# Kernel optimization log

Measured on AMD Instinct MI355X. Metric: run time of the kernel, lower is better.

Reference implementation:

```python
import jax, jax.numpy as jnp
import numpy as np

B, C_IN, C_OUT, N, L = 4, 128, 256, 4096, 4
D = C_OUT // 4
EPS_BN = 1e-5


def setup_inputs() -> dict:
    key = jax.random.key(0)
    ks = jax.random.split(key, 16)
    s_in = 1.0 / np.sqrt(C_IN)
    s_out = 1.0 / np.sqrt(C_OUT)
    return {
        "features": jax.random.normal(ks[0], (B, C_IN, N), dtype=jnp.float32),
        # LBR: conv1x1 -> BN -> ReLU -> conv1x1 -> BN -> ReLU
        "lbr_w1": jax.random.uniform(ks[1], (C_OUT, C_IN), jnp.float32, -s_in, s_in),
        "lbr_g1": jnp.ones((C_OUT,), jnp.float32),
        "lbr_b1": jnp.zeros((C_OUT,), jnp.float32),
        "lbr_w2": jax.random.uniform(ks[2], (C_OUT, C_OUT), jnp.float32, -s_out, s_out),
        "lbr_g2": jnp.ones((C_OUT,), jnp.float32),
        "lbr_b2": jnp.zeros((C_OUT,), jnp.float32),
        # per-layer OffsetAttention params (stacked on leading L axis)
        # q_conv and k_conv share the same weight (q_conv.weight = k_conv.weight)
        "attn_qk_w": jax.random.uniform(ks[3], (L, D, C_OUT), jnp.float32, -s_out, s_out),
        "attn_v_w": jax.random.uniform(ks[4], (L, C_OUT, C_OUT), jnp.float32, -s_out, s_out),
        "attn_v_b": jax.random.uniform(ks[5], (L, C_OUT), jnp.float32, -s_out, s_out),
        "attn_t_w": jax.random.uniform(ks[6], (L, C_OUT, C_OUT), jnp.float32, -s_out, s_out),
        "attn_t_b": jax.random.uniform(ks[7], (L, C_OUT), jnp.float32, -s_out, s_out),
        "attn_bn_g": jnp.ones((L, C_OUT), jnp.float32),
        "attn_bn_b": jnp.zeros((L, C_OUT), jnp.float32),
    }


def batchnorm1d(x, gamma, beta):
    # x: [B, C, N]; training-mode BN: batch stats over (B, N), biased variance
    mean = jnp.mean(x, axis=(0, 2), keepdims=True)
    var = jnp.mean(jnp.square(x - mean), axis=(0, 2), keepdims=True)
    xn = (x - mean) * jax.lax.rsqrt(var + EPS_BN)
    return xn * gamma[None, :, None] + beta[None, :, None]


def offset_attention(x, qk_w, v_w, v_b, t_w, t_b, bn_g, bn_b):
    # x: [B, C, N]
    K = jnp.einsum("dc,bcn->bdn", qk_w, x)            # [B, D, N]
    # Q = same conv, permuted to [B, N, D]; attention_map = Q @ K -> [B, N, N]
    attn = jnp.einsum("bdn,bdm->bnm", K, K)
    attn = jax.nn.softmax(attn, axis=-1)
    # extra L1 renorm over dim=1 (column-wise)
    attn = attn / (1e-9 + jnp.sum(attn, axis=1, keepdims=True))
    V = jnp.einsum("dc,bcn->bdn", v_w, x) + v_b[None, :, None]  # [B, C, N]
    new_feat = jnp.einsum("bcn,bnm->bcm", V, attn)    # [B, C, N]
    off = x - new_feat
    t = jnp.einsum("dc,bcn->bdn", t_w, off) + t_b[None, :, None]
    return jax.nn.relu(batchnorm1d(t, bn_g, bn_b))


def reference(features, lbr_w1, lbr_g1, lbr_b1, lbr_w2, lbr_g2, lbr_b2,
              attn_qk_w, attn_v_w, attn_v_b, attn_t_w, attn_t_b,
              attn_bn_g, attn_bn_b):
    # LBR stem
    h = jnp.einsum("dc,bcn->bdn", lbr_w1, features)
    h = jax.nn.relu(batchnorm1d(h, lbr_g1, lbr_b1))
    h = jnp.einsum("dc,bcn->bdn", lbr_w2, h)
    h = jax.nn.relu(batchnorm1d(h, lbr_g2, lbr_b2))
    # stacked offset attention; output concatenates attention outputs only
    outs = []
    cur = h
    for i in range(L):
        cur = offset_attention(cur, attn_qk_w[i], attn_v_w[i], attn_v_b[i],
                               attn_t_w[i], attn_t_b[i], attn_bn_g[i], attn_bn_b[i])
        outs.append(cur)
    return jnp.concatenate(outs, axis=1)  # [B, C_OUT*L, N]
```

## Files before the change

kernel.cpp:

```cpp
#include <hip/hip_runtime.h>
#include <hip/hip_bf16.h>
#include <math.h>

#define NPTS 4096
#define CO   256
#define CI   128
#define BB   4
#define DQ   64
#define LL   4
#define PST  136

typedef __attribute__((ext_vector_type(8))) short bf16x8;
typedef __attribute__((ext_vector_type(4))) float f32x4;

#define MFMA16(a,b,c) __builtin_amdgcn_mfma_f32_16x16x32_bf16((a),(b),(c),0,0,0)

__device__ __forceinline__ short fb(float x) {
  __hip_bfloat16 h = __float2bfloat16(x);
  return __builtin_bit_cast(short, h);
}
__device__ __forceinline__ float bf(short s) {
  unsigned u = ((unsigned)(unsigned short)s) << 16;
  return __builtin_bit_cast(float, u);
}

__global__ __launch_bounds__(256) void cvtw_k(
    const float* __restrict__ S, short* __restrict__ D, int n8)
{
  const int i = blockIdx.x * 256 + threadIdx.x;
  if (i < n8) {
    const float4 a = ((const float4*)S)[i * 2];
    const float4 b = ((const float4*)S)[i * 2 + 1];
    bf16x8 r;
    r[0] = fb(a.x); r[1] = fb(a.y); r[2] = fb(a.z); r[3] = fb(a.w);
    r[4] = fb(b.x); r[5] = fb(b.y); r[6] = fb(b.z); r[7] = fb(b.w);
    ((bf16x8*)D)[i] = r;
  }
}

__global__ __launch_bounds__(256) void tcvt_k(
    const float* __restrict__ X, long xbs, int C, short* __restrict__ XT)
{
  const int n0 = blockIdx.x * 64, c0 = blockIdx.y * 64, b = blockIdx.z;
  const int t = threadIdx.x, tl = t & 63, tg = t >> 6;
  __shared__ float xs[64][65];
#pragma unroll
  for (int r = 0; r < 16; ++r) {
    const int cc = tg * 16 + r;
    xs[cc][tl] = X[(long)b * xbs + (long)(c0 + cc) * NPTS + n0 + tl];
  }
  __syncthreads();
#pragma unroll
  for (int r = 0; r < 16; ++r) {
    const int nn = tg * 16 + r;
    XT[((long)b * NPTS + n0 + nn) * C + c0 + tl] = fb(xs[tl][nn]);
  }
}

template<int OMODE, bool BIAS>
__global__ __launch_bounds__(256) void conv_a(
    const short* __restrict__ XT, int C,
    const short* __restrict__ Wb, const float* __restrict__ bias,
    void* __restrict__ Yv, long ybs)
{
  const int n0 = blockIdx.x * 128, d0 = blockIdx.y * 64, b = blockIdx.z;
  const int tid = threadIdx.x, w = tid >> 6, l = tid & 63, lg = l >> 4, lr = l & 15;
  const short* xb = XT + (long)b * NPTS * C;
  f32x4 acc[8];
#pragma unroll
  for (int i = 0; i < 8; ++i) acc[i] = (f32x4){0.f, 0.f, 0.f, 0.f};
  const int dr = d0 + w * 16 + lr;
  for (int kc = 0; kc < C; kc += 32) {
    const bf16x8 af = *(const bf16x8*)&Wb[(long)dr * C + kc + lg * 8];
#pragma unroll
    for (int ni = 0; ni < 8; ++ni) {
      const bf16x8 bx = *(const bf16x8*)&xb[(long)(n0 + ni * 16 + lr) * C + kc + lg * 8];
      acc[ni] = MFMA16(af, bx, acc[ni]);
    }
  }
  float bv[4] = {0.f, 0.f, 0.f, 0.f};
  if (BIAS) {
    const float4 b4 = *(const float4*)&bias[d0 + w * 16 + lg * 4];
    bv[0] = b4.x; bv[1] = b4.y; bv[2] = b4.z; bv[3] = b4.w;
  }
  const int db = d0 + w * 16 + lg * 4;
#pragma unroll
  for (int ni = 0; ni < 8; ++ni) {
    const int n = n0 + ni * 16 + lr;
#pragma unroll
    for (int j = 0; j < 4; ++j) {
      const float o = acc[ni][j] + bv[j];
      if constexpr (OMODE == 0) {
        ((float*)Yv)[(long)b * ybs + (long)(db + j) * NPTS + n] = o;
      } else {
        ((short*)Yv)[(long)b * ybs + ((long)(n0 >> 7) * CO + db + j) * 128 + (n & 127)] = fb(o);
      }
    }
  }
}

__global__ __launch_bounds__(256) void conv_b(
    const short* __restrict__ XT, const short* __restrict__ Wb,
    short* __restrict__ KTo)
{
  const int n0 = blockIdx.x * 64, b = blockIdx.y;
  const int tid = threadIdx.x, w = tid >> 6, l = tid & 63, lg = l >> 4, lr = l & 15;
  const short* xb = XT + (long)b * NPTS * CO;
  f32x4 acc[4];
#pragma unroll
  for (int i = 0; i < 4; ++i) acc[i] = (f32x4){0.f, 0.f, 0.f, 0.f};
  const long nr = n0 + w * 16 + lr;
  for (int kc = 0; kc < CO; kc += 32) {
    const bf16x8 af = *(const bf16x8*)&xb[nr * CO + kc + lg * 8];
#pragma unroll
    for (int di = 0; di < 4; ++di) {
      const bf16x8 wf = *(const bf16x8*)&Wb[(long)(di * 16 + lr) * CO + kc + lg * 8];
      acc[di] = MFMA16(af, wf, acc[di]);
    }
  }
  short* Ko = KTo + (long)b * NPTS * DQ;
  const int nb = n0 + w * 16 + lg * 4;
#pragma unroll
  for (int j = 0; j < 4; ++j) {
#pragma unroll
    for (int di = 0; di < 4; ++di)
      Ko[(long)(nb + j) * DQ + di * 16 + lr] = fb(acc[di][j]);
  }
}

__global__ __launch_bounds__(256) void bnstats_k(
    const float* __restrict__ X, long xbs,
    float* __restrict__ mean, float* __restrict__ rstd)
{
  const int c = blockIdx.x, t = threadIdx.x;
  float s = 0.f, s2 = 0.f;
  for (int b = 0; b < BB; ++b) {
    const float4* p = (const float4*)(X + (long)b * xbs + (long)c * NPTS);
    for (int n = t; n < NPTS / 4; n += 256) {
      const float4 v = p[n];
      s  += v.x + v.y + v.z + v.w;
      s2 += v.x * v.x + v.y * v.y + v.z * v.z + v.w * v.w;
    }
  }
#pragma unroll
  for (int o = 32; o > 0; o >>= 1) { s += __shfl_down(s, o); s2 += __shfl_down(s2, o); }
  __shared__ float a1[4], a2[4];
  if ((t & 63) == 0) { a1[t >> 6] = s; a2[t >> 6] = s2; }
  __syncthreads();
  if (t == 0) {
    const float S  = a1[0] + a1[1] + a1[2] + a1[3];
    const float S2 = a2[0] + a2[1] + a2[2] + a2[3];
    const float m  = S / (float)(BB * NPTS);
    const float v  = S2 / (float)(BB * NPTS) - m * m;
    mean[c] = m;
    rstd[c] = rsqrtf(v + 1e-5f);
  }
}

template<bool WF32, bool WBF>
__global__ __launch_bounds__(256) void bnrelu_t(
    const float* __restrict__ X, long xbs,
    const float* __restrict__ mean, const float* __restrict__ rstd,
    const float* __restrict__ g, const float* __restrict__ be,
    float* __restrict__ Yf, long ybs, short* __restrict__ XT)
{
  const int n0 = blockIdx.x * 64, c0 = blockIdx.y * 64, b = blockIdx.z;
  const int t = threadIdx.x, tl = t & 63, tg = t >> 6;
  __shared__ float xs[64][65];
#pragma unroll
  for (int r = 0; r < 16; ++r) {
    const int cc = tg * 16 + r, c = c0 + cc;
    float v = X[(long)b * xbs + (long)c * NPTS + n0 + tl];
    v = fmaxf((v - mean[c]) * rstd[c] * g[c] + be[c], 0.f);
    if (WF32) Yf[(long)b * ybs + (long)c * NPTS + n0 + tl] = v;
    xs[cc][tl] = v;
  }
  __syncthreads();
  if (WBF) {
#pragma unroll
    for (int r = 0; r < 16; ++r) {
      const int nn = tg * 16 + r;
      XT[((long)b * NPTS + n0 + nn) * CO + c0 + tl] = fb(xs[tl][nn]);
    }
  }
}

#define ONL(MX, SM, SV) { const float m2_ = fmaxf(MX, SV); \
  SM = SM * __expf(MX - m2_) + __expf(SV - m2_); MX = m2_; }
#define MRG(MX, SM, OFF) { const float om_ = __shfl_xor(MX, OFF); \
  const float os_ = __shfl_xor(SM, OFF); \
  const float m2_ = fmaxf(MX, om_); \
  SM = SM * __expf(MX - m2_) + os_ * __expf(om_ - m2_); MX = m2_; }

__global__ __launch_bounds__(256) void rowstats_mfma(
    const short* __restrict__ KT, float* __restrict__ pmax, float* __restrict__ psum)
{
  const int bid = blockIdx.x;
  const int b = (bid >> 1) & 3;
  const int idx = (bid >> 3) * 2 + (bid & 1);
  const int n0 = (idx & 63) * 64;
  const int chunk = idx >> 6;
  const int tid = threadIdx.x, w = tid >> 6, l = tid & 63, lg = l >> 4, lr = l & 15;
  const short* Kb = KT + (long)b * NPTS * DQ;
  const int nr = n0 + w * 16 + lr;
  const bf16x8 a0 = *(const bf16x8*)&Kb[(long)nr * DQ + lg * 8];
  const bf16x8 a1 = *(const bf16x8*)&Kb[(long)nr * DQ + 32 + lg * 8];

  float mx0 = -INFINITY, mx1 = -INFINITY, mx2 = -INFINITY, mx3 = -INFINITY;
  float sm0 = 0.f, sm1 = 0.f, sm2 = 0.f, sm3 = 0.f;

  const int mc = chunk * (NPTS / 4);
  for (int m0 = mc; m0 < mc + NPTS / 4; m0 += 16) {
    const bf16x8 b0 = *(const bf16x8*)&Kb[(long)(m0 + lr) * DQ + lg * 8];
    const bf16x8 b1 = *(const bf16x8*)&Kb[(long)(m0 + lr) * DQ + 32 + lg * 8];
    f32x4 s = {0.f, 0.f, 0.f, 0.f};
    s = MFMA16(a0, b0, s);
    s = MFMA16(a1, b1, s);
    ONL(mx0, sm0, s[0]); ONL(mx1, sm1, s[1]);
    ONL(mx2, sm2, s[2]); ONL(mx3, sm3, s[3]);
  }
#pragma unroll
  for (int off = 1; off < 16; off <<= 1) {
    MRG(mx0, sm0, off); MRG(mx1, sm1, off);
    MRG(mx2, sm2, off); MRG(mx3, sm3, off);
  }
  if (lr == 0) {
    const long base = ((long)chunk * BB + b) * NPTS + n0 + w * 16 + lg * 4;
    pmax[base + 0] = mx0; pmax[base + 1] = mx1; pmax[base + 2] = mx2; pmax[base + 3] = mx3;
    psum[base + 0] = sm0; psum[base + 1] = sm1; psum[base + 2] = sm2; psum[base + 3] = sm3;
  }
}

__global__ __launch_bounds__(256) void combine_k(
    const float* __restrict__ pmax, const float* __restrict__ psum,
    float* __restrict__ rmax, float* __restrict__ rinv)
{
  const long i = (long)blockIdx.x * 256 + threadIdx.x;
  const long st = (long)BB * NPTS;
  float m = pmax[i];
  m = fmaxf(m, pmax[st + i]); m = fmaxf(m, pmax[2 * st + i]); m = fmaxf(m, pmax[3 * st + i]);
  const float s = psum[i] * __expf(pmax[i] - m)
                + psum[st + i] * __expf(pmax[st + i] - m)
                + psum[2 * st + i] * __expf(pmax[2 * st + i] - m)
                + psum[3 * st + i] * __expf(pmax[3 * st + i] - m);
  rmax[i] = m;
  rinv[i] = 1.f / s;
}

__global__ __launch_bounds__(512) void pass2_mfma(
    const short* __restrict__ KT, const short* __restrict__ Vblk,
    const float* __restrict__ rmax, const float* __restrict__ rinv,
    short* __restrict__ XO)
{
  const int bid = blockIdx.x;
  const int b  = (bid >> 1) & 3;
  const int m0 = ((bid >> 3) * 2 + (bid & 1)) * 64;
  const int tid = threadIdx.x;
  const int w = tid >> 6, l = tid & 63, lg = l >> 4, lr = l & 15;

  const short* Kb = KT + (long)b * NPTS * DQ;
  const short* Vb = Vblk + (long)b * CO * NPTS;
  const float* rmb = rmax + (long)b * NPTS;
  const float* rib = rinv + (long)b * NPTS;

  __shared__ short Ps[2][64][PST];
  __shared__ float cspart[8][64];
  __shared__ float csum[64];

  bf16x8 bK[4][2];
#pragma unroll
  for (int ms = 0; ms < 4; ++ms) {
    bK[ms][0] = *(const bf16x8*)&Kb[(long)(m0 + ms * 16 + lr) * DQ + lg * 8];
    bK[ms][1] = *(const bf16x8*)&Kb[(long)(m0 + ms * 16 + lr) * DQ + 32 + lg * 8];
  }

  f32x4 acc[4][2];
#pragma unroll
  for (int i = 0; i < 4; ++i) {
    acc[i][0] = (f32x4){0.f, 0.f, 0.f, 0.f};
    acc[i][1] = (f32x4){0.f, 0.f, 0.f, 0.f};
  }
  float cs[4] = {0.f, 0.f, 0.f, 0.f};
  const int c0 = w * 32;
  const int nb = w * 16;

  bf16x8 a0 = *(const bf16x8*)&Kb[(long)(nb + lr) * DQ + lg * 8];
  bf16x8 a1 = *(const bf16x8*)&Kb[(long)(nb + lr) * DQ + 32 + lg * 8];
  float4 rm4 = *(const float4*)&rmb[nb + lg * 4];
  float4 ri4 = *(const float4*)&rib[nb + lg * 4];

  int buf = 0;
  for (int n0 = 0; n0 < NPTS; n0 += 128) {
    const short* vt = Vb + (long)(n0 >> 7) * CO * 128;
    bf16x8 vf[4][2];
#pragma unroll
    for (int kc = 0; kc < 4; ++kc) {
      vf[kc][0] = *(const bf16x8*)&vt[(long)(c0 + lr) * 128 + kc * 32 + lg * 8];
      vf[kc][1] = *(const bf16x8*)&vt[(long)(c0 + 16 + lr) * 128 + kc * 32 + lg * 8];
    }
    f32x4 s[4];
#pragma unroll
    for (int ms = 0; ms < 4; ++ms) {
      s[ms] = (f32x4){0.f, 0.f, 0.f, 0.f};
      s[ms] = MFMA16(a0, bK[ms][0], s[ms]);
      s[ms] = MFMA16(a1, bK[ms][1], s[ms]);
    }
#pragma unroll
    for (int ms = 0; ms < 4; ++ms) {
      const float p0 = __expf(s[ms][0] - rm4.x) * ri4.x;
      const float p1 = __expf(s[ms][1] - rm4.y) * ri4.y;
      const float p2 = __expf(s[ms][2] - rm4.z) * ri4.z;
      const float p3 = __expf(s[ms][3] - rm4.w) * ri4.w;
      cs[ms] += p0 + p1 + p2 + p3;
      const unsigned u0 = ((unsigned)(unsigned short)fb(p1) << 16) | (unsigned short)fb(p0);
      const unsigned u1 = ((unsigned)(unsigned short)fb(p3) << 16) | (unsigned short)fb(p2);
      *(uint2*)&Ps[buf][ms * 16 + lr][nb + lg * 4] = make_uint2(u0, u1);
    }
    asm volatile("s_waitcnt lgkmcnt(0)" ::: "memory");
    __builtin_amdgcn_s_barrier();
    if (n0 + 128 < NPTS) {
      a0 = *(const bf16x8*)&Kb[(long)(n0 + 128 + nb + lr) * DQ + lg * 8];
      a1 = *(const bf16x8*)&Kb[(long)(n0 + 128 + nb + lr) * DQ + 32 + lg * 8];
      rm4 = *(const float4*)&rmb[n0 + 128 + nb + lg * 4];
      ri4 = *(const float4*)&rib[n0 + 128 + nb + lg * 4];
    }
#pragma unroll
    for (int kc = 0; kc < 4; ++kc) {
      bf16x8 pa[4];
#pragma unroll
      for (int ms = 0; ms < 4; ++ms)
        pa[ms] = *(const bf16x8*)&Ps[buf][ms * 16 + lr][kc * 32 + lg * 8];
#pragma unroll
      for (int ms = 0; ms < 4; ++ms) {
        acc[ms][0] = MFMA16(pa[ms], vf[kc][0], acc[ms][0]);
        acc[ms][1] = MFMA16(pa[ms], vf[kc][1], acc[ms][1]);
      }
    }
    buf ^= 1;
  }

  __syncthreads();
#pragma unroll
  for (int ms = 0; ms < 4; ++ms) {
    float csv = cs[ms];
    csv += __shfl_xor(csv, 16); csv += __shfl_xor(csv, 32);
    if (lg == 0) cspart[w][ms * 16 + lr] = csv;
  }
  __syncthreads();
  if (tid < 64) {
    float s = 0.f;
#pragma unroll
    for (int ww = 0; ww < 8; ++ww) s += cspart[ww][tid];
    csum[tid] = s;
  }
  __syncthreads();

  short* XOb = XO + (long)b * NPTS * CO;
#pragma unroll
  for (int ms = 0; ms < 4; ++ms) {
#pragma unroll
    for (int j = 0; j < 4; ++j) {
      const int m = m0 + ms * 16 + lg * 4 + j;
      const float inv = 1.f / (1e-9f + csum[ms * 16 + lg * 4 + j]);
      const long i0 = (long)m * CO + c0 + lr;
      const long i1 = (long)m * CO + c0 + 16 + lr;
      XOb[i0] = fb(bf(XOb[i0]) - acc[ms][0][j] * inv);
      XOb[i1] = fb(bf(XOb[i1]) - acc[ms][1][j] * inv);
    }
  }
}

extern "C" void kernel_launch(void* const* d_in, const int* in_sizes, int n_in,
                              void* d_out, int out_size, void* d_ws, size_t ws_size,
                              hipStream_t stream)
{
  const float* feat = (const float*)d_in[0];
  const float* w1   = (const float*)d_in[1];
  const float* g1   = (const float*)d_in[2];
  const float* b1   = (const float*)d_in[3];
  const float* w2   = (const float*)d_in[4];
  const float* g2   = (const float*)d_in[5];
  const float* b2   = (const float*)d_in[6];
  const float* qkw  = (const float*)d_in[7];
  const float* vw   = (const float*)d_in[8];
  const float* vb   = (const float*)d_in[9];
  const float* tw   = (const float*)d_in[10];
  const float* tb   = (const float*)d_in[11];
  const float* bng  = (const float*)d_in[12];
  const float* bnb  = (const float*)d_in[13];

  float* out = (float*)d_out;

  short* xt    = (short*)d_ws;
  short* KTb   = xt + (long)BB * NPTS * CO;
  short* Vblk  = KTb + (long)BB * NPTS * DQ;
  short* wb1   = Vblk + (long)BB * CO * NPTS;
  short* wb2   = wb1 + (long)CO * CI;
  short* wqk   = wb2 + (long)CO * CO;
  short* wv    = wqk + (long)LL * DQ * CO;
  short* wt    = wv + (long)LL * CO * CO;
  float* pmaxb = (float*)(wt + (long)LL * CO * CO);
  float* psumb = pmaxb + (long)4 * BB * NPTS;
  float* rmaxb = psumb + (long)4 * BB * NPTS;
  float* rinvb = rmaxb + (long)BB * NPTS;
  float* meanb = rinvb + (long)BB * NPTS;
  float* rstdb = meanb + CO;

  const long OBS = (long)LL * CO * NPTS;
  float* h1 = out + (long)2 * CO * NPTS;
  float* x0 = out + (long)1 * CO * NPTS;

  const dim3 blk(256);

  cvtw_k<<<dim3((CO * CI / 8 + 255) / 256), blk, 0, stream>>>(w1, wb1, CO * CI / 8);
  cvtw_k<<<dim3((CO * CO / 8 + 255) / 256), blk, 0, stream>>>(w2, wb2, CO * CO / 8);
  cvtw_k<<<dim3((LL * DQ * CO / 8 + 255) / 256), blk, 0, stream>>>(qkw, wqk, LL * DQ * CO / 8);
  cvtw_k<<<dim3((LL * CO * CO / 8 + 255) / 256), blk, 0, stream>>>(vw, wv, LL * CO * CO / 8);
  cvtw_k<<<dim3((LL * CO * CO / 8 + 255) / 256), blk, 0, stream>>>(tw, wt, LL * CO * CO / 8);

  tcvt_k<<<dim3(64, 2, BB), blk, 0, stream>>>(feat, (long)CI * NPTS, CI, xt);
  conv_a<0, false><<<dim3(32, 4, BB), blk, 0, stream>>>(xt, CI, wb1, nullptr, h1, OBS);
  bnstats_k<<<dim3(CO), blk, 0, stream>>>(h1, OBS, meanb, rstdb);
  bnrelu_t<false, true><<<dim3(64, 4, BB), blk, 0, stream>>>(
      h1, OBS, meanb, rstdb, g1, b1, nullptr, 0, xt);
  conv_a<0, false><<<dim3(32, 4, BB), blk, 0, stream>>>(xt, CO, wb2, nullptr, x0, OBS);
  bnstats_k<<<dim3(CO), blk, 0, stream>>>(x0, OBS, meanb, rstdb);
  bnrelu_t<false, true><<<dim3(64, 4, BB), blk, 0, stream>>>(
      x0, OBS, meanb, rstdb, g2, b2, nullptr, 0, xt);

  for (int lyr = 0; lyr < LL; ++lyr) {
    float* nft = out + (long)lyr * CO * NPTS;
    conv_b<<<dim3(64, BB), blk, 0, stream>>>(xt, wqk + (long)lyr * DQ * CO, KTb);
    conv_a<1, true><<<dim3(32, 4, BB), blk, 0, stream>>>(
        xt, CO, wv + (long)lyr * CO * CO, vb + (long)lyr * CO, Vblk, (long)CO * NPTS);
    rowstats_mfma<<<dim3(1024), blk, 0, stream>>>(KTb, pmaxb, psumb);
    combine_k<<<dim3(BB * NPTS / 256), blk, 0, stream>>>(pmaxb, psumb, rmaxb, rinvb);
    pass2_mfma<<<dim3(256), dim3(512), 0, stream>>>(KTb, Vblk, rmaxb, rinvb, xt);
    conv_a<0, true><<<dim3(32, 4, BB), blk, 0, stream>>>(
        xt, CO, wt + (long)lyr * CO * CO, tb + (long)lyr * CO, nft, OBS);
    bnstats_k<<<dim3(CO), blk, 0, stream>>>(nft, OBS, meanb, rstdb);
    if (lyr < LL - 1) {
      bnrelu_t<true, true><<<dim3(64, 4, BB), blk, 0, stream>>>(
          nft, OBS, meanb, rstdb, bng + (long)lyr * CO, bnb + (long)lyr * CO, nft, OBS, xt);
    } else {
      bnrelu_t<true, false><<<dim3(64, 4, BB), blk, 0, stream>>>(
          nft, OBS, meanb, rstdb, bng + (long)lyr * CO, bnb + (long)lyr * CO, nft, OBS, nullptr);
    }
  }
}
```

Baseline: 911.2 us.

## Fuse BN stats into conv epilogue, bf16 intermediates, two-pass rowstats, merged weight cast

Merges the five weight-conversion launches into one kernel. The 1x1 conv now writes its pre-BN output as bf16 into scratch and accumulates per-channel sum and sum-of-squares partials in its epilogue. A small finisher kernel reduces those partials, replacing the full-tensor bnstats pass. The conv tile is halved to 64 points to give more blocks. The row-softmax statistics kernel switches from online max/sum to two passes, recomputing QK^T to drop the per-element rescale exps. This trades extra MFMA work and bf16 rounding of pre-BN values for less memory traffic and fewer launches.

```diff
diff --git a/kernel.cpp b/kernel.cpp
--- a/kernel.cpp
+++ b/kernel.cpp
@@ -24,18 +24,27 @@
   return __builtin_bit_cast(float, u);
 }
 
-__global__ __launch_bounds__(256) void cvtw_k(
-    const float* __restrict__ S, short* __restrict__ D, int n8)
-{
-  const int i = blockIdx.x * 256 + threadIdx.x;
-  if (i < n8) {
-    const float4 a = ((const float4*)S)[i * 2];
-    const float4 b = ((const float4*)S)[i * 2 + 1];
-    bf16x8 r;
-    r[0] = fb(a.x); r[1] = fb(a.y); r[2] = fb(a.z); r[3] = fb(a.w);
-    r[4] = fb(b.x); r[5] = fb(b.y); r[6] = fb(b.z); r[7] = fb(b.w);
-    ((bf16x8*)D)[i] = r;
-  }
+__global__ __launch_bounds__(256) void cvt5_k(
+    const float* __restrict__ s1, short* __restrict__ d1, int n1,
+    const float* __restrict__ s2, short* __restrict__ d2, int n2,
+    const float* __restrict__ s3, short* __restrict__ d3, int n3,
+    const float* __restrict__ s4, short* __restrict__ d4, int n4,
+    const float* __restrict__ s5, short* __restrict__ d5, int n5)
+{
+  int i = blockIdx.x * 256 + threadIdx.x;
+  const float* S; short* D;
+  if      (i < n1)                       { S = s1; D = d1; }
+  else if ((i -= n1) < n2)               { S = s2; D = d2; }
+  else if ((i -= n2) < n3)               { S = s3; D = d3; }
+  else if ((i -= n3) < n4)               { S = s4; D = d4; }
+  else if ((i -= n4) < n5)               { S = s5; D = d5; }
+  else return;
+  const float4 a = ((const float4*)S)[i * 2];
+  const float4 b = ((const float4*)S)[i * 2 + 1];
+  bf16x8 r;
+  r[0] = fb(a.x); r[1] = fb(a.y); r[2] = fb(a.z); r[3] = fb(a.w);
+  r[4] = fb(b.x); r[5] = fb(b.y); r[6] = fb(b.z); r[7] = fb(b.w);
+  ((bf16x8*)D)[i] = r;
 }
 
 __global__ __launch_bounds__(256) void tcvt_k(
@@ -61,19 +70,20 @@
 __global__ __launch_bounds__(256) void conv_a(
     const short* __restrict__ XT, int C,
     const short* __restrict__ Wb, const float* __restrict__ bias,
-    void* __restrict__ Yv, long ybs)
-{
-  const int n0 = blockIdx.x * 128, d0 = blockIdx.y * 64, b = blockIdx.z;
+    short* __restrict__ Yv, long ybs,
+    float* __restrict__ ps1, float* __restrict__ ps2)
+{
+  const int n0 = blockIdx.x * 64, d0 = blockIdx.y * 64, b = blockIdx.z;
   const int tid = threadIdx.x, w = tid >> 6, l = tid & 63, lg = l >> 4, lr = l & 15;
   const short* xb = XT + (long)b * NPTS * C;
-  f32x4 acc[8];
-#pragma unroll
-  for (int i = 0; i < 8; ++i) acc[i] = (f32x4){0.f, 0.f, 0.f, 0.f};
+  f32x4 acc[4];
+#pragma unroll
+  for (int i = 0; i < 4; ++i) acc[i] = (f32x4){0.f, 0.f, 0.f, 0.f};
   const int dr = d0 + w * 16 + lr;
   for (int kc = 0; kc < C; kc += 32) {
     const bf16x8 af = *(const bf16x8*)&Wb[(long)dr * C + kc + lg * 8];
 #pragma unroll
-    for (int ni = 0; ni < 8; ++ni) {
+    for (int ni = 0; ni < 4; ++ni) {
       const bf16x8 bx = *(const bf16x8*)&xb[(long)(n0 + ni * 16 + lr) * C + kc + lg * 8];
       acc[ni] = MFMA16(af, bx, acc[ni]);
     }
@@ -84,16 +94,39 @@
     bv[0] = b4.x; bv[1] = b4.y; bv[2] = b4.z; bv[3] = b4.w;
   }
   const int db = d0 + w * 16 + lg * 4;
-#pragma unroll
-  for (int ni = 0; ni < 8; ++ni) {
+  float s1[4], s2[4];
+#pragma unroll
+  for (int j = 0; j < 4; ++j) { s1[j] = 0.f; s2[j] = 0.f; }
+#pragma unroll
+  for (int ni = 0; ni < 4; ++ni) {
     const int n = n0 + ni * 16 + lr;
 #pragma unroll
     for (int j = 0; j < 4; ++j) {
-      const float o = acc[ni][j] + bv[j];
-      if constexpr (OMODE == 0) {
-        ((float*)Yv)[(long)b * ybs + (long)(db + j) * NPTS + n] = o;
+      const short ob = fb(acc[ni][j] + bv[j]);
+      if constexpr (OMODE == 1) {
+        Yv[(long)b * ybs + ((long)(n >> 7) * CO + db + j) * 128 + (n & 127)] = ob;
       } else {
-        ((short*)Yv)[(long)b * ybs + ((long)(n0 >> 7) * CO + db + j) * 128 + (n & 127)] = fb(o);
+        Yv[(long)b * ybs + (long)(db + j) * NPTS + n] = ob;
+        const float o = bf(ob);
+        s1[j] += o; s2[j] += o * o;
+      }
+    }
+  }
+  if constexpr (OMODE == 2) {
+#pragma unroll
+    for (int j = 0; j < 4; ++j) {
+#pragma unroll
+      for (int off = 1; off < 16; off <<= 1) {
+        s1[j] += __shfl_xor(s1[j], off);
+        s2[j] += __shfl_xor(s2[j], off);
+      }
+    }
+    if (lr == 0) {
+      const int slot = b * 64 + blockIdx.x;
+#pragma unroll
+      for (int j = 0; j < 4; ++j) {
+        ps1[(long)(db + j) * 256 + slot] = s1[j];
+        ps2[(long)(db + j) * 256 + slot] = s2[j];
       }
     }
   }
@@ -128,30 +161,22 @@
   }
 }
 
-__global__ __launch_bounds__(256) void bnstats_k(
-    const float* __restrict__ X, long xbs,
+__global__ __launch_bounds__(64) void bnfin_k(
+    const float* __restrict__ ps1, const float* __restrict__ ps2,
     float* __restrict__ mean, float* __restrict__ rstd)
 {
   const int c = blockIdx.x, t = threadIdx.x;
   float s = 0.f, s2 = 0.f;
-  for (int b = 0; b < BB; ++b) {
-    const float4* p = (const float4*)(X + (long)b * xbs + (long)c * NPTS);
-    for (int n = t; n < NPTS / 4; n += 256) {
-      const float4 v = p[n];
-      s  += v.x + v.y + v.z + v.w;
-      s2 += v.x * v.x + v.y * v.y + v.z * v.z + v.w * v.w;
-    }
+#pragma unroll
+  for (int i = 0; i < 4; ++i) {
+    s  += ps1[(long)c * 256 + t + i * 64];
+    s2 += ps2[(long)c * 256 + t + i * 64];
   }
 #pragma unroll
   for (int o = 32; o > 0; o >>= 1) { s += __shfl_down(s, o); s2 += __shfl_down(s2, o); }
-  __shared__ float a1[4], a2[4];
-  if ((t & 63) == 0) { a1[t >> 6] = s; a2[t >> 6] = s2; }
-  __syncthreads();
   if (t == 0) {
-    const float S  = a1[0] + a1[1] + a1[2] + a1[3];
-    const float S2 = a2[0] + a2[1] + a2[2] + a2[3];
-    const float m  = S / (float)(BB * NPTS);
-    const float v  = S2 / (float)(BB * NPTS) - m * m;
+    const float m = s / (float)(BB * NPTS);
+    const float v = s2 / (float)(BB * NPTS) - m * m;
     mean[c] = m;
     rstd[c] = rsqrtf(v + 1e-5f);
   }
@@ -159,7 +184,7 @@
 
 template<bool WF32, bool WBF>
 __global__ __launch_bounds__(256) void bnrelu_t(
-    const float* __restrict__ X, long xbs,
+    const short* __restrict__ X, long xbs,
     const float* __restrict__ mean, const float* __restrict__ rstd,
     const float* __restrict__ g, const float* __restrict__ be,
     float* __restrict__ Yf, long ybs, short* __restrict__ XT)
@@ -170,7 +195,7 @@
 #pragma unroll
   for (int r = 0; r < 16; ++r) {
     const int cc = tg * 16 + r, c = c0 + cc;
-    float v = X[(long)b * xbs + (long)c * NPTS + n0 + tl];
+    float v = bf(X[(long)b * xbs + (long)c * NPTS + n0 + tl]);
     v = fmaxf((v - mean[c]) * rstd[c] * g[c] + be[c], 0.f);
     if (WF32) Yf[(long)b * ybs + (long)c * NPTS + n0 + tl] = v;
     xs[cc][tl] = v;
@@ -184,13 +209,6 @@
     }
   }
 }
-
-#define ONL(MX, SM, SV) { const float m2_ = fmaxf(MX, SV); \
-  SM = SM * __expf(MX - m2_) + __expf(SV - m2_); MX = m2_; }
-#define MRG(MX, SM, OFF) { const float om_ = __shfl_xor(MX, OFF); \
-  const float os_ = __shfl_xor(SM, OFF); \
-  const float m2_ = fmaxf(MX, om_); \
-  SM = SM * __expf(MX - m2_) + os_ * __expf(om_ - m2_); MX = m2_; }
 
 __global__ __launch_bounds__(256) void rowstats_mfma(
     const short* __restrict__ KT, float* __restrict__ pmax, float* __restrict__ psum)
@@ -205,29 +223,56 @@
   const int nr = n0 + w * 16 + lr;
   const bf16x8 a0 = *(const bf16x8*)&Kb[(long)nr * DQ + lg * 8];
   const bf16x8 a1 = *(const bf16x8*)&Kb[(long)nr * DQ + 32 + lg * 8];
-
-  float mx0 = -INFINITY, mx1 = -INFINITY, mx2 = -INFINITY, mx3 = -INFINITY;
-  float sm0 = 0.f, sm1 = 0.f, sm2 = 0.f, sm3 = 0.f;
-
   const int mc = chunk * (NPTS / 4);
-  for (int m0 = mc; m0 < mc + NPTS / 4; m0 += 16) {
-    const bf16x8 b0 = *(const bf16x8*)&Kb[(long)(m0 + lr) * DQ + lg * 8];
-    const bf16x8 b1 = *(const bf16x8*)&Kb[(long)(m0 + lr) * DQ + 32 + lg * 8];
-    f32x4 s = {0.f, 0.f, 0.f, 0.f};
-    s = MFMA16(a0, b0, s);
-    s = MFMA16(a1, b1, s);
-    ONL(mx0, sm0, s[0]); ONL(mx1, sm1, s[1]);
-    ONL(mx2, sm2, s[2]); ONL(mx3, sm3, s[3]);
-  }
-#pragma unroll
-  for (int off = 1; off < 16; off <<= 1) {
-    MRG(mx0, sm0, off); MRG(mx1, sm1, off);
-    MRG(mx2, sm2, off); MRG(mx3, sm3, off);
-  }
+
+  float mx[4][4];
+#pragma unroll
+  for (int p = 0; p < 4; ++p)
+#pragma unroll
+    for (int j = 0; j < 4; ++j) mx[p][j] = -INFINITY;
+  for (int m0 = mc; m0 < mc + NPTS / 4; m0 += 64) {
+#pragma unroll
+    for (int p = 0; p < 4; ++p) {
+      const bf16x8 b0 = *(const bf16x8*)&Kb[(long)(m0 + p * 16 + lr) * DQ + lg * 8];
+      const bf16x8 b1 = *(const bf16x8*)&Kb[(long)(m0 + p * 16 + lr) * DQ + 32 + lg * 8];
+      f32x4 s = {0.f, 0.f, 0.f, 0.f};
+      s = MFMA16(a0, b0, s);
+      s = MFMA16(a1, b1, s);
+#pragma unroll
+      for (int j = 0; j < 4; ++j) mx[p][j] = fmaxf(mx[p][j], s[j]);
+    }
+  }
+  float mxf[4];
+#pragma unroll
+  for (int j = 0; j < 4; ++j)
+    mxf[j] = fmaxf(fmaxf(mx[0][j], mx[1][j]), fmaxf(mx[2][j], mx[3][j]));
+#pragma unroll
+  for (int off = 1; off < 16; off <<= 1)
+#pragma unroll
+    for (int j = 0; j < 4; ++j) mxf[j] = fmaxf(mxf[j], __shfl_xor(mxf[j], off));
+
+  float sm[4] = {0.f, 0.f, 0.f, 0.f};
+  for (int m0 = mc; m0 < mc + NPTS / 4; m0 += 64) {
+#pragma unroll
+    for (int p = 0; p < 4; ++p) {
+      const bf16x8 b0 = *(const bf16x8*)&Kb[(long)(m0 + p * 16 + lr) * DQ + lg * 8];
+      const bf16x8 b1 = *(const bf16x8*)&Kb[(long)(m0 + p * 16 + lr) * DQ + 32 + lg * 8];
+      f32x4 s = {0.f, 0.f, 0.f, 0.f};
+      s = MFMA16(a0, b0, s);
+      s = MFMA16(a1, b1, s);
+#pragma unroll
+      for (int j = 0; j < 4; ++j) sm[j] += __expf(s[j] - mxf[j]);
+    }
+  }
+#pragma unroll
+  for (int off = 1; off < 16; off <<= 1)
+#pragma unroll
+    for (int j = 0; j < 4; ++j) sm[j] += __shfl_xor(sm[j], off);
+
   if (lr == 0) {
     const long base = ((long)chunk * BB + b) * NPTS + n0 + w * 16 + lg * 4;
-    pmax[base + 0] = mx0; pmax[base + 1] = mx1; pmax[base + 2] = mx2; pmax[base + 3] = mx3;
-    psum[base + 0] = sm0; psum[base + 1] = sm1; psum[base + 2] = sm2; psum[base + 3] = sm3;
+#pragma unroll
+    for (int j = 0; j < 4; ++j) { pmax[base + j] = mxf[j]; psum[base + j] = sm[j]; }
   }
 }
 
@@ -319,8 +364,8 @@
     asm volatile("s_waitcnt lgkmcnt(0)" ::: "memory");
     __builtin_amdgcn_s_barrier();
     if (n0 + 128 < NPTS) {
-      a0 = *(const bf16x8*)&Kb[(long)(n0 + 128 + nb + lr) * DQ + lg * 8];
-      a1 = *(const bf16x8*)&Kb[(long)(n0 + 128 + nb + lr) * DQ + 32 + lg * 8];
+      a0  = *(const bf16x8*)&Kb[(long)(n0 + 128 + nb + lr) * DQ + lg * 8];
+      a1  = *(const bf16x8*)&Kb[(long)(n0 + 128 + nb + lr) * DQ + 32 + lg * 8];
       rm4 = *(const float4*)&rmb[n0 + 128 + nb + lg * 4];
       ri4 = *(const float4*)&rib[n0 + 128 + nb + lg * 4];
     }
@@ -403,48 +448,54 @@
   float* psumb = pmaxb + (long)4 * BB * NPTS;
   float* rmaxb = psumb + (long)4 * BB * NPTS;
   float* rinvb = rmaxb + (long)BB * NPTS;
-  float* meanb = rinvb + (long)BB * NPTS;
+  float* ps1   = rinvb + (long)BB * NPTS;
+  float* ps2   = ps1 + (long)CO * 256;
+  float* meanb = ps2 + (long)CO * 256;
   float* rstdb = meanb + CO;
 
   const long OBS = (long)LL * CO * NPTS;
-  float* h1 = out + (long)2 * CO * NPTS;
-  float* x0 = out + (long)1 * CO * NPTS;
+  const long TBS = (long)CO * NPTS;
+  short* pre = Vblk;
 
   const dim3 blk(256);
 
-  cvtw_k<<<dim3((CO * CI / 8 + 255) / 256), blk, 0, stream>>>(w1, wb1, CO * CI / 8);
-  cvtw_k<<<dim3((CO * CO / 8 + 255) / 256), blk, 0, stream>>>(w2, wb2, CO * CO / 8);
-  cvtw_k<<<dim3((LL * DQ * CO / 8 + 255) / 256), blk, 0, stream>>>(qkw, wqk, LL * DQ * CO / 8);
-  cvtw_k<<<dim3((LL * CO * CO / 8 + 255) / 256), blk, 0, stream>>>(vw, wv, LL * CO * CO / 8);
-  cvtw_k<<<dim3((LL * CO * CO / 8 + 255) / 256), blk, 0, stream>>>(tw, wt, LL * CO * CO / 8);
+  {
+    const int n1 = CO * CI / 8, n2 = CO * CO / 8, n3 = LL * DQ * CO / 8,
+              n4 = LL * CO * CO / 8, n5 = LL * CO * CO / 8;
+    const int tot = n1 + n2 + n3 + n4 + n5;
+    cvt5_k<<<dim3((tot + 255) / 256), blk, 0, stream>>>(
+        w1, wb1, n1, w2, wb2, n2, qkw, wqk, n3, vw, wv, n4, tw, wt, n5);
+  }
 
   tcvt_k<<<dim3(64, 2, BB), blk, 0, stream>>>(feat, (long)CI * NPTS, CI, xt);
-  conv_a<0, false><<<dim3(32, 4, BB), blk, 0, stream>>>(xt, CI, wb1, nullptr, h1, OBS);
-  bnstats_k<<<dim3(CO), blk, 0, stream>>>(h1, OBS, meanb, rstdb);
+  conv_a<2, false><<<dim3(64, 4, BB), blk, 0, stream>>>(
+      xt, CI, wb1, nullptr, pre, TBS, ps1, ps2);
+  bnfin_k<<<dim3(CO), dim3(64), 0, stream>>>(ps1, ps2, meanb, rstdb);
   bnrelu_t<false, true><<<dim3(64, 4, BB), blk, 0, stream>>>(
-      h1, OBS, meanb, rstdb, g1, b1, nullptr, 0, xt);
-  conv_a<0, false><<<dim3(32, 4, BB), blk, 0, stream>>>(xt, CO, wb2, nullptr, x0, OBS);
-  bnstats_k<<<dim3(CO), blk, 0, stream>>>(x0, OBS, meanb, rstdb);
+      pre, TBS, meanb, rstdb, g1, b1, nullptr, 0, xt);
+  conv_a<2, false><<<dim3(64, 4, BB), blk, 0, stream>>>(
+      xt, CO, wb2, nullptr, pre, TBS, ps1, ps2);
+  bnfin_k<<<dim3(CO), dim3(64), 0, stream>>>(ps1, ps2, meanb, rstdb);
   bnrelu_t<false, true><<<dim3(64, 4, BB), blk, 0, stream>>>(
-      x0, OBS, meanb, rstdb, g2, b2, nullptr, 0, xt);
+      pre, TBS, meanb, rstdb, g2, b2, nullptr, 0, xt);
 
   for (int lyr = 0; lyr < LL; ++lyr) {
     float* nft = out + (long)lyr * CO * NPTS;
     conv_b<<<dim3(64, BB), blk, 0, stream>>>(xt, wqk + (long)lyr * DQ * CO, KTb);
-    conv_a<1, true><<<dim3(32, 4, BB), blk, 0, stream>>>(
-        xt, CO, wv + (long)lyr * CO * CO, vb + (long)lyr * CO, Vblk, (long)CO * NPTS);
+    conv_a<1, true><<<dim3(64, 4, BB), blk, 0, stream>>>(
+        xt, CO, wv + (long)lyr * CO * CO, vb + (long)lyr * CO, Vblk, TBS, nullptr, nullptr);
     rowstats_mfma<<<dim3(1024), blk, 0, stream>>>(KTb, pmaxb, psumb);
     combine_k<<<dim3(BB * NPTS / 256), blk, 0, stream>>>(pmaxb, psumb, rmaxb, rinvb);
     pass2_mfma<<<dim3(256), dim3(512), 0, stream>>>(KTb, Vblk, rmaxb, rinvb, xt);
-    conv_a<0, true><<<dim3(32, 4, BB), blk, 0, stream>>>(
-        xt, CO, wt + (long)lyr * CO * CO, tb + (long)lyr * CO, nft, OBS);
-    bnstats_k<<<dim3(CO), blk, 0, stream>>>(nft, OBS, meanb, rstdb);
+    conv_a<2, true><<<dim3(64, 4, BB), blk, 0, stream>>>(
+        xt, CO, wt + (long)lyr * CO * CO, tb + (long)lyr * CO, pre, TBS, ps1, ps2);
+    bnfin_k<<<dim3(CO), dim3(64), 0, stream>>>(ps1, ps2, meanb, rstdb);
     if (lyr < LL - 1) {
       bnrelu_t<true, true><<<dim3(64, 4, BB), blk, 0, stream>>>(
-          nft, OBS, meanb, rstdb, bng + (long)lyr * CO, bnb + (long)lyr * CO, nft, OBS, xt);
+          pre, TBS, meanb, rstdb, bng + (long)lyr * CO, bnb + (long)lyr * CO, nft, OBS, xt);
     } else {
       bnrelu_t<true, false><<<dim3(64, 4, BB), blk, 0, stream>>>(
-          nft, OBS, meanb, rstdb, bng + (long)lyr * CO, bnb + (long)lyr * CO, nft, OBS, nullptr);
-    }
-  }
-}
+          pre, TBS, meanb, rstdb, bng + (long)lyr * CO, bnb + (long)lyr * CO, nft, OBS, nullptr);
+    }
+  }
+}
```

Result: slower. 1.109 ms (+21.7%).
